# Optimization experiments

Hardware: AMD Instinct MI355X
Metric: run time of the kernel (lower is better)

## Reference

```python
import jax, jax.numpy as jnp
import numpy as np

N = 50000
D = 256
K = 16  # fixed neighbor-list degree (regularized form of the ragged edge_dict)


def setup_inputs() -> dict:
    key = jax.random.key(0)
    k1, k2, k3, k4 = jax.random.split(key, 4)
    feats = jax.random.normal(k1, (N, D), dtype=jnp.float32)
    edge_dict = jax.random.randint(k2, (N, K), 0, N)  # int32 neighbor indices
    W = jax.random.normal(k3, (D, D), dtype=jnp.float32) * (1.0 / np.sqrt(D))
    b = jax.random.normal(k4, (D,), dtype=jnp.float32) * 0.01
    idx = jnp.arange(N)
    sadj = jnp.zeros((1,), dtype=jnp.float32)
    epoch = 0
    return {"idx": idx, "feats": feats, "edge_dict": edge_dict,
            "sadj": sadj, "epoch": epoch, "W": W, "b": b}


def reference(idx, feats, edge_dict, sadj, epoch, W, b):
    # fc -> relu (dropout is identity in eval mode; p=0.5 train-only)
    x = jax.nn.relu(feats @ W.T + b)  # [N, D]
    # region_aggregate: per-node mean over fixed-degree neighbor lists
    pooled = jnp.mean(x[edge_dict], axis=1)  # gather [N, K, D] -> mean -> [N, D]
    return pooled
```

## Files before the change

### kernel.cpp

```cpp
#include <hip/hip_runtime.h>
#include <hip/hip_bf16.h>

#define NN  50000
#define DD  256
#define KNB 16
#define BM  32
#define NSL 8
#define SLW 32
#define NKT 8
#define NGRP ((NN + 63) / 64)
#define NB32 ((NN + 31) / 32)

typedef __attribute__((ext_vector_type(8))) short bf16x8;
typedef __attribute__((ext_vector_type(4))) float f32x4;
typedef __attribute__((ext_vector_type(4))) int   i32x4;

static __device__ __forceinline__ float bf2f(unsigned int u16) {
    union { unsigned int i; float f; } c; c.i = u16 << 16; return c.f;
}
static __device__ __forceinline__ float bf2f_hi(unsigned int u) {
    union { unsigned int i; float f; } c; c.i = u & 0xffff0000u; return c.f;
}
static __device__ __forceinline__ short f2bf(float f) {
    union { float f; unsigned int i; } c; c.f = f;
    unsigned int r = c.i + 0x7FFFu + ((c.i >> 16) & 1u);
    return (short)(r >> 16);
}
static __device__ __forceinline__ bf16x8 pack8(float4 a, float4 b) {
    union { __hip_bfloat162 h[4]; bf16x8 v; } u;
    u.h[0] = __float22bfloat162_rn(make_float2(a.x, a.y));
    u.h[1] = __float22bfloat162_rn(make_float2(a.z, a.w));
    u.h[2] = __float22bfloat162_rn(make_float2(b.x, b.y));
    u.h[3] = __float22bfloat162_rn(make_float2(b.z, b.w));
    return u.v;
}

#define GLOAD_LDS16(g, l) \
    __builtin_amdgcn_global_load_lds((const __attribute__((address_space(1))) unsigned int*)(g), \
                                     (__attribute__((address_space(3))) unsigned int*)(l), 16, 0, 0)

__global__ void convert_w(const float* __restrict__ W, unsigned short* __restrict__ Wbf)
{
    int s = blockIdx.x * blockDim.x + threadIdx.x;
    if (s >= 8192) return;
    int j  = s & 15;
    int kb = (s >> 4) & 3;
    int nb = (s >> 6) & 15;
    int kt = s >> 10;
    const float4* p = (const float4*)(W + (nb * 16 + j) * DD + kt * 32 + kb * 8);
    *(bf16x8*)&Wbf[(size_t)s * 8] = pack8(p[0], p[1]);
}

__global__ __launch_bounds__(256, 3) void gemm_relu(
    const float* __restrict__ feats, const unsigned short* __restrict__ Wbf,
    const float* __restrict__ bias, unsigned short* __restrict__ xs)
{
    __shared__ short At[8192];
    __shared__ short Wt[2][8192];

    const int tid  = threadIdx.x;
    const int lane = tid & 63;
    const int wc   = tid >> 6;
    const int l15  = lane & 15;
    const int lg   = lane >> 4;
    const int blockRow = blockIdx.x * BM;

    auto wstage = [&](int kt, int buf) {
        const char* src = (const char*)Wbf + kt * 16384 + tid * 16;
        char* dst = (char*)&Wt[buf][0] + tid * 16;
        #pragma unroll
        for (int c = 0; c < 4; ++c)
            GLOAD_LDS16(src + c * 4096, dst + c * 4096);
    };

    wstage(0, 0);
    {
        const int r = tid >> 3, q = tid & 7;
        int row = blockRow + r; if (row > NN - 1) row = NN - 1;
        const float* base = feats + (size_t)row * DD + q * 32;
        const int m = r >> 4, i15 = r & 15;
        #pragma unroll
        for (int kq = 0; kq < 4; ++kq) {
            float4 lo = *(const float4*)(base + kq * 8);
            float4 hi = *(const float4*)(base + kq * 8 + 4);
            int slot = (((q * 2 + m) * 4 + kq) * 16 + i15) * 8;
            *(bf16x8*)&At[slot] = pack8(lo, hi);
        }
    }

    float bv[4];
    #pragma unroll
    for (int n = 0; n < 4; ++n) bv[n] = bias[wc * 64 + n * 16 + l15];

    f32x4 acc[2][4];
    #pragma unroll
    for (int m = 0; m < 2; ++m)
        #pragma unroll
        for (int n = 0; n < 4; ++n) acc[m][n] = (f32x4)0.0f;

    __syncthreads();

    #pragma unroll
    for (int kt = 0; kt < NKT; ++kt) {
        const int cur = kt & 1;
        if (kt + 1 < NKT) wstage(kt + 1, cur ^ 1);

        bf16x8 afr[2], bfr[4];
        #pragma unroll
        for (int m = 0; m < 2; ++m)
            afr[m] = *(const bf16x8*)&At[(((kt * 2 + m) * 4 + lg) * 16 + l15) * 8];
        #pragma unroll
        for (int n = 0; n < 4; ++n)
            bfr[n] = *(const bf16x8*)&Wt[cur][(((wc * 4 + n) * 4 + lg) * 16 + l15) * 8];

        #pragma unroll
        for (int m = 0; m < 2; ++m)
            #pragma unroll
            for (int n = 0; n < 4; ++n)
                acc[m][n] = __builtin_amdgcn_mfma_f32_16x16x32_bf16(
                    afr[m], bfr[n], acc[m][n], 0, 0, 0);

        __syncthreads();
    }

    #pragma unroll
    for (int n = 0; n < 4; ++n) {
        const int sl = wc * 2 + (n >> 1);
        const int c  = (n & 1) * 16 + l15;
        unsigned short* xb = xs + (size_t)sl * NN * SLW + c;
        #pragma unroll
        for (int m = 0; m < 2; ++m) {
            int rbase = blockRow + m * 16 + (lg << 2);
            f32x4 a = acc[m][n];
            #pragma unroll
            for (int r = 0; r < 4; ++r) {
                int row = rbase + r;
                if (row < NN) {
                    float vv = fmaxf(a[r] + bv[n], 0.0f);
                    xb[(size_t)row * SLW] = (unsigned short)f2bf(vv);
                }
            }
        }
    }
}

__global__ __launch_bounds__(256) void gather_mean(
    const int* __restrict__ edge, const unsigned short* __restrict__ xs,
    float* __restrict__ out)
{
    const int s    = blockIdx.x & 7;
    const int lane = threadIdx.x & 63;
    const int w    = threadIdx.x >> 6;
    const int g    = lane >> 2, q = lane & 3;
    const unsigned short* xsl = xs + (size_t)s * NN * SLW;
    const unsigned qo = q * 8;

    for (int grp = blockIdx.x >> 3; grp < NGRP; grp += 256) {
        const int iw0 = grp * 64 + w * 16;
        const int i   = iw0 + g;

        int eoff = iw0 * KNB + lane * 4;
        if (eoff > NN * KNB - 4) eoff = NN * KNB - 4;
        i32x4 e4 = *(const i32x4*)(edge + eoff);
        int e[4] = { e4[0], e4[1], e4[2], e4[3] };

        float a[8];
        #pragma unroll
        for (int j = 0; j < 8; ++j) a[j] = 0.0f;

        #pragma unroll
        for (int k = 0; k < KNB; ++k) {
            int src = (lane & 60) | (k >> 2);
            unsigned n = (unsigned)__shfl(e[k & 3], src, 64);
            bf16x8 v = *(const bf16x8*)(xsl + n * SLW + qo);
            const unsigned int* vu = (const unsigned int*)&v;
            #pragma unroll
            for (int j = 0; j < 4; ++j) {
                a[2 * j]     += bf2f(vu[j] & 0xffffu);
                a[2 * j + 1] += bf2f_hi(vu[j]);
            }
        }

        if (i < NN) {
            f32x4 o0 = { a[0] * 0.0625f, a[1] * 0.0625f, a[2] * 0.0625f, a[3] * 0.0625f };
            f32x4 o1 = { a[4] * 0.0625f, a[5] * 0.0625f, a[6] * 0.0625f, a[7] * 0.0625f };
            float* op = out + (size_t)i * DD + s * SLW + q * 8;
            __builtin_nontemporal_store(o0, (f32x4*)op);
            __builtin_nontemporal_store(o1, (f32x4*)(op + 4));
        }
    }
}

extern "C" void kernel_launch(void* const* d_in, const int* in_sizes, int n_in,
                              void* d_out, int out_size, void* d_ws, size_t ws_size,
                              hipStream_t stream) {
    const float* feats = (const float*)d_in[1];
    const int*   edge  = (const int*)d_in[2];
    const float* W     = (const float*)d_in[5];
    const float* b     = (const float*)d_in[6];
    float* out = (float*)d_out;

    unsigned short* xs  = (unsigned short*)d_ws;
    unsigned short* Wbf = (unsigned short*)((char*)d_ws + (size_t)NN * DD * 2);

    convert_w<<<dim3(32), dim3(256), 0, stream>>>(W, Wbf);
    gemm_relu<<<dim3(NB32), dim3(256), 0, stream>>>(feats, Wbf, b, xs);
    gather_mean<<<dim3(2048), dim3(256), 0, stream>>>(edge, xs, out);
}
```

Before: 68.55 us.

## Widen GEMM blocks to 512 threads and flatten gather grid with batched loads

The GEMM kernel now uses 512 threads (8 waves) per 32-row block, so each wave computes a 32x32 output tile instead of 32x64. Staging work and the A-tile conversion are split across more threads, and each wave writes one 32-column slice. The gather kernel drops its grid-stride loop and launches one block per 64-node group per slice. It also issues 8 neighbor loads before accumulating, to raise memory-level parallelism. Costs are more blocks, more barrier participants per block, and higher register use for the buffered loads.

```diff
diff --git a/kernel.cpp b/kernel.cpp
--- a/kernel.cpp
+++ b/kernel.cpp
@@ -51,7 +51,7 @@
     *(bf16x8*)&Wbf[(size_t)s * 8] = pack8(p[0], p[1]);
 }
 
-__global__ __launch_bounds__(256, 3) void gemm_relu(
+__global__ __launch_bounds__(512, 6) void gemm_relu(
     const float* __restrict__ feats, const unsigned short* __restrict__ Wbf,
     const float* __restrict__ bias, unsigned short* __restrict__ xs)
 {
@@ -68,35 +68,36 @@
     auto wstage = [&](int kt, int buf) {
         const char* src = (const char*)Wbf + kt * 16384 + tid * 16;
         char* dst = (char*)&Wt[buf][0] + tid * 16;
-        #pragma unroll
-        for (int c = 0; c < 4; ++c)
-            GLOAD_LDS16(src + c * 4096, dst + c * 4096);
+        GLOAD_LDS16(src, dst);
+        GLOAD_LDS16(src + 8192, dst + 8192);
     };
 
     wstage(0, 0);
     {
-        const int r = tid >> 3, q = tid & 7;
+        const int r = tid >> 4, c16 = tid & 15;
         int row = blockRow + r; if (row > NN - 1) row = NN - 1;
-        const float* base = feats + (size_t)row * DD + q * 32;
+        const float* base = feats + (size_t)row * DD + c16 * 16;
         const int m = r >> 4, i15 = r & 15;
-        #pragma unroll
-        for (int kq = 0; kq < 4; ++kq) {
-            float4 lo = *(const float4*)(base + kq * 8);
-            float4 hi = *(const float4*)(base + kq * 8 + 4);
-            int slot = (((q * 2 + m) * 4 + kq) * 16 + i15) * 8;
-            *(bf16x8*)&At[slot] = pack8(lo, hi);
-        }
-    }
-
-    float bv[4];
-    #pragma unroll
-    for (int n = 0; n < 4; ++n) bv[n] = bias[wc * 64 + n * 16 + l15];
-
-    f32x4 acc[2][4];
+        const int kt = c16 >> 1, kq0 = (c16 & 1) * 2;
+        float4 a0 = *(const float4*)(base);
+        float4 a1 = *(const float4*)(base + 4);
+        float4 a2 = *(const float4*)(base + 8);
+        float4 a3 = *(const float4*)(base + 12);
+        int s0 = (((kt * 2 + m) * 4 + kq0) * 16 + i15) * 8;
+        int s1 = (((kt * 2 + m) * 4 + kq0 + 1) * 16 + i15) * 8;
+        *(bf16x8*)&At[s0] = pack8(a0, a1);
+        *(bf16x8*)&At[s1] = pack8(a2, a3);
+    }
+
+    float bv[2];
+    #pragma unroll
+    for (int n = 0; n < 2; ++n) bv[n] = bias[wc * 32 + n * 16 + l15];
+
+    f32x4 acc[2][2];
     #pragma unroll
     for (int m = 0; m < 2; ++m)
         #pragma unroll
-        for (int n = 0; n < 4; ++n) acc[m][n] = (f32x4)0.0f;
+        for (int n = 0; n < 2; ++n) acc[m][n] = (f32x4)0.0f;
 
     __syncthreads();
 
@@ -105,29 +106,28 @@
         const int cur = kt & 1;
         if (kt + 1 < NKT) wstage(kt + 1, cur ^ 1);
 
-        bf16x8 afr[2], bfr[4];
+        bf16x8 afr[2], bfr[2];
         #pragma unroll
         for (int m = 0; m < 2; ++m)
             afr[m] = *(const bf16x8*)&At[(((kt * 2 + m) * 4 + lg) * 16 + l15) * 8];
         #pragma unroll
-        for (int n = 0; n < 4; ++n)
-            bfr[n] = *(const bf16x8*)&Wt[cur][(((wc * 4 + n) * 4 + lg) * 16 + l15) * 8];
+        for (int n = 0; n < 2; ++n)
+            bfr[n] = *(const bf16x8*)&Wt[cur][(((wc * 2 + n) * 4 + lg) * 16 + l15) * 8];
 
         #pragma unroll
         for (int m = 0; m < 2; ++m)
             #pragma unroll
-            for (int n = 0; n < 4; ++n)
+            for (int n = 0; n < 2; ++n)
                 acc[m][n] = __builtin_amdgcn_mfma_f32_16x16x32_bf16(
                     afr[m], bfr[n], acc[m][n], 0, 0, 0);
 
         __syncthreads();
     }
 
-    #pragma unroll
-    for (int n = 0; n < 4; ++n) {
-        const int sl = wc * 2 + (n >> 1);
-        const int c  = (n & 1) * 16 + l15;
-        unsigned short* xb = xs + (size_t)sl * NN * SLW + c;
+    unsigned short* xb = xs + (size_t)wc * NN * SLW;
+    #pragma unroll
+    for (int n = 0; n < 2; ++n) {
+        const int c = n * 16 + l15;
         #pragma unroll
         for (int m = 0; m < 2; ++m) {
             int rbase = blockRow + m * 16 + (lg << 2);
@@ -137,7 +137,7 @@
                 int row = rbase + r;
                 if (row < NN) {
                     float vv = fmaxf(a[r] + bv[n], 0.0f);
-                    xb[(size_t)row * SLW] = (unsigned short)f2bf(vv);
+                    xb[(size_t)row * SLW + c] = (unsigned short)f2bf(vv);
                 }
             }
         }
@@ -149,45 +149,52 @@
     float* __restrict__ out)
 {
     const int s    = blockIdx.x & 7;
+    const int grp  = blockIdx.x >> 3;
     const int lane = threadIdx.x & 63;
     const int w    = threadIdx.x >> 6;
     const int g    = lane >> 2, q = lane & 3;
+    const int iw0  = grp * 64 + w * 16;
+    const int i    = iw0 + g;
+
+    int eoff = iw0 * KNB + lane * 4;
+    if (eoff > NN * KNB - 4) eoff = NN * KNB - 4;
+    i32x4 e4 = *(const i32x4*)(edge + eoff);
+    int e[4] = { e4[0], e4[1], e4[2], e4[3] };
+
     const unsigned short* xsl = xs + (size_t)s * NN * SLW;
     const unsigned qo = q * 8;
 
-    for (int grp = blockIdx.x >> 3; grp < NGRP; grp += 256) {
-        const int iw0 = grp * 64 + w * 16;
-        const int i   = iw0 + g;
-
-        int eoff = iw0 * KNB + lane * 4;
-        if (eoff > NN * KNB - 4) eoff = NN * KNB - 4;
-        i32x4 e4 = *(const i32x4*)(edge + eoff);
-        int e[4] = { e4[0], e4[1], e4[2], e4[3] };
-
-        float a[8];
-        #pragma unroll
-        for (int j = 0; j < 8; ++j) a[j] = 0.0f;
-
-        #pragma unroll
-        for (int k = 0; k < KNB; ++k) {
+    float a[8];
+    #pragma unroll
+    for (int j = 0; j < 8; ++j) a[j] = 0.0f;
+
+    #pragma unroll
+    for (int half = 0; half < 2; ++half) {
+        bf16x8 vbuf[8];
+        #pragma unroll
+        for (int kk = 0; kk < 8; ++kk) {
+            int k = half * 8 + kk;
             int src = (lane & 60) | (k >> 2);
             unsigned n = (unsigned)__shfl(e[k & 3], src, 64);
-            bf16x8 v = *(const bf16x8*)(xsl + n * SLW + qo);
-            const unsigned int* vu = (const unsigned int*)&v;
+            vbuf[kk] = *(const bf16x8*)(xsl + n * SLW + qo);
+        }
+        #pragma unroll
+        for (int kk = 0; kk < 8; ++kk) {
+            const unsigned int* vu = (const unsigned int*)&vbuf[kk];
             #pragma unroll
             for (int j = 0; j < 4; ++j) {
                 a[2 * j]     += bf2f(vu[j] & 0xffffu);
                 a[2 * j + 1] += bf2f_hi(vu[j]);
             }
         }
-
-        if (i < NN) {
-            f32x4 o0 = { a[0] * 0.0625f, a[1] * 0.0625f, a[2] * 0.0625f, a[3] * 0.0625f };
-            f32x4 o1 = { a[4] * 0.0625f, a[5] * 0.0625f, a[6] * 0.0625f, a[7] * 0.0625f };
-            float* op = out + (size_t)i * DD + s * SLW + q * 8;
-            __builtin_nontemporal_store(o0, (f32x4*)op);
-            __builtin_nontemporal_store(o1, (f32x4*)(op + 4));
-        }
+    }
+
+    if (i < NN) {
+        f32x4 o0 = { a[0] * 0.0625f, a[1] * 0.0625f, a[2] * 0.0625f, a[3] * 0.0625f };
+        f32x4 o1 = { a[4] * 0.0625f, a[5] * 0.0625f, a[6] * 0.0625f, a[7] * 0.0625f };
+        float* op = out + (size_t)i * DD + s * SLW + q * 8;
+        __builtin_nontemporal_store(o0, (f32x4*)op);
+        __builtin_nontemporal_store(o1, (f32x4*)(op + 4));
     }
 }
 
@@ -204,6 +211,6 @@
     unsigned short* Wbf = (unsigned short*)((char*)d_ws + (size_t)NN * DD * 2);
 
     convert_w<<<dim3(32), dim3(256), 0, stream>>>(W, Wbf);
-    gemm_relu<<<dim3(NB32), dim3(256), 0, stream>>>(feats, Wbf, b, xs);
-    gather_mean<<<dim3(2048), dim3(256), 0, stream>>>(edge, xs, out);
-}
+    gemm_relu<<<dim3(NB32), dim3(512), 0, stream>>>(feats, Wbf, b, xs);
+    gather_mean<<<dim3(NGRP * NSL), dim3(256), 0, stream>>>(edge, xs, out);
+}
```

After: 65.25 us. 4.8% less time.
